# Optimization experiments

Hardware: AMD Instinct MI355X
Metric: run time of the kernel (lower is better)

Reference implementation:

```python
import jax, jax.numpy as jnp
import numpy as np

B, S, D, H = 4, 2048, 512, 8
DH = D // H


def setup_inputs() -> dict:
    key = jax.random.key(0)
    ks = jax.random.split(key, 7)
    scale = 1.0 / np.sqrt(DH)  # mimic nn.Linear init magnitude
    return {
        "x": jax.random.normal(ks[0], (B, S, D), dtype=jnp.float32),
        "Wq": jax.random.normal(ks[1], (H, DH, DH), dtype=jnp.float32) * scale,
        "bq": jax.random.normal(ks[2], (H, DH), dtype=jnp.float32) * scale,
        "Wk": jax.random.normal(ks[3], (H, DH, DH), dtype=jnp.float32) * scale,
        "bk": jax.random.normal(ks[4], (H, DH), dtype=jnp.float32) * scale,
        "Wv": jax.random.normal(ks[5], (H, DH, DH), dtype=jnp.float32) * scale,
        "bv": jax.random.normal(ks[6], (H, DH), dtype=jnp.float32) * scale,
    }


def reference(x, Wq, bq, Wk, bk, Wv, bv):
    # x: [B, S, D] -> per-head slices [B, S, H, DH] (contiguous chunks, as in torch slicing)
    xh = x.reshape(B, S, H, DH)
    # nn.Linear: y = x @ W.T + b, per head. Wq[h] is [out, in].
    q = jnp.einsum("bshd,hed->bshe", xh, Wq) + bq  # [B, S, H, DH]
    k = jnp.einsum("bshd,hed->bshe", xh, Wk) + bk
    v = jnp.einsum("bshd,hed->bshe", xh, Wv) + bv
    scores = jnp.einsum("bshe,bthe->bhst", q, k) / jnp.sqrt(jnp.float32(DH))  # [B, H, S, S]
    attn = jax.nn.softmax(scores, axis=-1)
    out = jnp.einsum("bhst,bthe->bshe", attn, v)  # [B, S, H, DH]
    return out.reshape(B, S, D)  # hstack of head outputs == concat along feature dim
```

## Files before the change

### kernel.cpp

```cpp
#include <hip/hip_runtime.h>
#include <math.h>

#define B_ 4
#define S_ 2048
#define D_ 512
#define H_ 8
#define DH_ 64
#define BH_ (B_*H_)
#define SCALE 0.1803368801111243f

typedef __attribute__((ext_vector_type(4)))  float f32x4;
typedef __attribute__((ext_vector_type(16))) float f32x16;
typedef __attribute__((ext_vector_type(8)))  short bf16x8;
typedef __attribute__((ext_vector_type(4)))  uint  u32x4;

__device__ inline uint rnepk(float a, float b) {
    uint ua = __builtin_bit_cast(uint, a), ub = __builtin_bit_cast(uint, b);
    ua += 0x7FFFu + ((ua >> 16) & 1u);
    ub += 0x7FFFu + ((ub >> 16) & 1u);
    return (ua >> 16) | (ub & 0xFFFF0000u);
}
__device__ inline uint truncpk(float lo, float hi) {
    return __builtin_amdgcn_perm(__builtin_bit_cast(uint, hi),
                                 __builtin_bit_cast(uint, lo), 0x07060302u);
}
__device__ inline f32x16 zero16() {
    f32x16 z;
    #pragma unroll
    for (int i = 0; i < 16; ++i) z[i] = 0.f;
    return z;
}
__device__ inline bf16x8 pack8(f32x4 a, f32x4 c) {
    u32x4 u;
    u.x = rnepk(a[0], a[1]); u.y = rnepk(a[2], a[3]);
    u.z = rnepk(c[0], c[1]); u.w = rnepk(c[2], c[3]);
    return __builtin_bit_cast(bf16x8, u);
}

#if __has_builtin(__builtin_amdgcn_permlane32_swap)
__device__ inline void lane32swap(uint& a, uint& b) {
    typedef __attribute__((ext_vector_type(2))) uint u32x2;
    u32x2 r = __builtin_amdgcn_permlane32_swap(a, b, false, false);
    a = r.x; b = r.y;
}
#else
__device__ inline void lane32swap(uint& a, uint& b) {
    const int l5 = (threadIdx.x & 63) >> 5;
    uint send = l5 ? a : b;
    uint recv = __shfl_xor(send, 32);
    uint an = l5 ? recv : a;
    uint bn = l5 ? b : recv;
    a = an; b = bn;
}
#endif

__global__ __launch_bounds__(256)
void prep_w(const float* __restrict__ Wq, const float* __restrict__ Wk,
            const float* __restrict__ Wv, ushort* __restrict__ Wf)
{
    const int pb = blockIdx.x;
    const int proj = pb >> 3, h = pb & 7;
    const float* W = (proj == 0 ? Wq : proj == 1 ? Wk : Wv) + h * DH_ * DH_;
    #pragma unroll
    for (int it = 0; it < 2; ++it) {
        const int slot = threadIdx.x + it * 256;
        const int c = slot >> 6, lane = slot & 63;
        const int l31 = lane & 31, l5 = lane >> 5;
        const int et = c >> 2, st = c & 3;
        const float* wr = W + (et * 32 + l31) * DH_ + st * 16 + l5 * 8;
        bf16x8 v = pack8(*(const f32x4*)wr, *(const f32x4*)(wr + 4));
        *(bf16x8*)(Wf + ((size_t)pb * 8 + c) * 512 + lane * 8) = v;
    }
}

__global__ __launch_bounds__(256, 2)
void qkv_mfma(const float* __restrict__ x,
              const float* __restrict__ bq, const float* __restrict__ bk,
              const float* __restrict__ bv, const ushort* __restrict__ Wf,
              ushort* __restrict__ Qf, ushort* __restrict__ Kf,
              ushort* __restrict__ Vf)
{
    const int bh = blockIdx.x, b = bh >> 3, h = bh & 7;
    const int sblk = blockIdx.y, s0 = sblk * 128;
    const int tid = threadIdx.x;
    const int w = tid >> 6, lane = tid & 63, l31 = lane & 31, l5 = lane >> 5;

    __shared__ __align__(16) ushort bnc[4][2560];
    __shared__ __align__(16) ushort vsh[64 * 136];
    ushort* mybnc = bnc[w];

    const ushort* wqb = Wf + ((size_t)(0 * 8 + h)) * 8 * 512;
    const ushort* wkb = Wf + ((size_t)(1 * 8 + h)) * 8 * 512;
    const ushort* wvb = Wf + ((size_t)(2 * 8 + h)) * 8 * 512;

    const int srow = w * 32 + l31;
    const float* xr = x + ((size_t)(b * S_ + s0 + srow)) * D_ + h * DH_;
    bf16x8 xf[4];
    #pragma unroll
    for (int st = 0; st < 4; ++st)
        xf[st] = pack8(*(const f32x4*)(xr + st * 16 + l5 * 8),
                       *(const f32x4*)(xr + st * 16 + l5 * 8 + 4));

    {
        bf16x8 wf[2][4];
        #pragma unroll
        for (int et = 0; et < 2; ++et)
            #pragma unroll
            for (int st = 0; st < 4; ++st)
                wf[et][st] = *(const bf16x8*)(wkb + (et * 4 + st) * 512 + lane * 8);
        #pragma unroll
        for (int et = 0; et < 2; ++et) {
            f32x16 acc = zero16();
            #pragma unroll
            for (int st = 0; st < 4; ++st)
                acc = __builtin_amdgcn_mfma_f32_32x32x16_bf16(wf[et][st], xf[st], acc, 0, 0, 0);
            #pragma unroll
            for (int rg = 0; rg < 4; ++rg) {
                float4 b4 = *(const float4*)(bk + h * DH_ + et * 32 + rg * 8 + l5 * 4);
                uint2 pk;
                pk.x = rnepk(acc[rg * 4 + 0] + b4.x, acc[rg * 4 + 1] + b4.y);
                pk.y = rnepk(acc[rg * 4 + 2] + b4.z, acc[rg * 4 + 3] + b4.w);
                *(uint2*)(mybnc + l31 * 72 + et * 32 + rg * 8 + l5 * 4) = pk;
            }
        }
        const int kt = sblk * 2 + (w >> 1), g = w & 1;
        ushort* kd = Kf + (((size_t)(bh * 32 + kt)) * 2 + g) * 2048;
        #pragma unroll
        for (int st = 0; st < 4; ++st) {
            uint4 v = *(const uint4*)(mybnc + l31 * 72 + st * 16 + l5 * 8);
            *(uint4*)(kd + st * 512 + lane * 8) = v;
        }
    }

    {
        bf16x8 wf[2][4];
        #pragma unroll
        for (int et = 0; et < 2; ++et)
            #pragma unroll
            for (int st = 0; st < 4; ++st)
                wf[et][st] = *(const bf16x8*)(wqb + (et * 4 + st) * 512 + lane * 8);
        #pragma unroll
        for (int et = 0; et < 2; ++et) {
            f32x16 acc = zero16();
            #pragma unroll
            for (int st = 0; st < 4; ++st)
                acc = __builtin_amdgcn_mfma_f32_32x32x16_bf16(wf[et][st], xf[st], acc, 0, 0, 0);
            #pragma unroll
            for (int rg = 0; rg < 4; ++rg) {
                float4 b4 = *(const float4*)(bq + h * DH_ + et * 32 + rg * 8 + l5 * 4);
                uint2 pk;
                pk.x = rnepk((acc[rg * 4 + 0] + b4.x) * SCALE, (acc[rg * 4 + 1] + b4.y) * SCALE);
                pk.y = rnepk((acc[rg * 4 + 2] + b4.z) * SCALE, (acc[rg * 4 + 3] + b4.w) * SCALE);
                *(uint2*)(mybnc + l31 * 72 + et * 32 + rg * 8 + l5 * 4) = pk;
            }
        }
        ushort* qd = Qf + ((size_t)(bh * 64 + sblk * 4 + w)) * 2048;
        #pragma unroll
        for (int st = 0; st < 4; ++st) {
            uint4 v = *(const uint4*)(mybnc + l31 * 72 + st * 16 + l5 * 8);
            *(uint4*)(qd + st * 512 + lane * 8) = v;
        }
    }

    {
        bf16x8 wf[2][4];
        #pragma unroll
        for (int et = 0; et < 2; ++et)
            #pragma unroll
            for (int st = 0; st < 4; ++st)
                wf[et][st] = *(const bf16x8*)(wvb + (et * 4 + st) * 512 + lane * 8);
        #pragma unroll
        for (int et = 0; et < 2; ++et) {
            f32x16 acc = zero16();
            #pragma unroll
            for (int st = 0; st < 4; ++st)
                acc = __builtin_amdgcn_mfma_f32_32x32x16_bf16(xf[st], wf[et][st], acc, 0, 0, 0);
            const float bb = bv[h * DH_ + et * 32 + l31];
            #pragma unroll
            for (int rg = 0; rg < 4; ++rg) {
                uint2 pk;
                pk.x = rnepk(acc[rg * 4 + 0] + bb, acc[rg * 4 + 1] + bb);
                pk.y = rnepk(acc[rg * 4 + 2] + bb, acc[rg * 4 + 3] + bb);
                *(uint2*)(vsh + (et * 32 + l31) * 136 + w * 32 + rg * 8 + l5 * 4) = pk;
            }
        }
        __syncthreads();
        #pragma unroll
        for (int i = 0; i < 4; ++i) {
            const int c = w * 4 + i;
            const int ktl = c >> 3, dht = (c >> 2) & 1, st = c & 3;
            uint4 v = *(const uint4*)(vsh + (dht * 32 + l31) * 136 + ktl * 64 + st * 16 + l5 * 8);
            *(uint4*)(Vf + (((size_t)(bh * 32 + sblk * 2 + ktl)) * 2 + dht) * 2048
                      + st * 512 + lane * 8) = v;
        }
    }
}

__global__ __launch_bounds__(256, 4)
void flash_mfma(const ushort* __restrict__ Qf, const ushort* __restrict__ Kf,
                const ushort* __restrict__ Vf, float* __restrict__ out)
{
    const int bh = blockIdx.x, qblk2 = blockIdx.y;
    const int b = bh >> 3, h = bh & 7;
    const int tid = threadIdx.x;
    const int w = tid >> 6, lane = tid & 63, l31 = lane & 31, l5 = lane >> 5;
    const int qh = w >> 1, p = w & 1;

    __shared__ __align__(16) float mb[2 * 32 * 68 + 64];

    const ushort* kbase = Kf + (size_t)bh * 32 * 4096;
    const ushort* vbase = Vf + (size_t)bh * 32 * 4096;

    bf16x8 qf[4];
    #pragma unroll
    for (int st = 0; st < 4; ++st)
        qf[st] = *(const bf16x8*)(Qf + ((size_t)(bh * 64 + qblk2 * 2 + qh)) * 2048
                                  + st * 512 + lane * 8);

    f32x16 O[2];
    O[0] = zero16(); O[1] = zero16();
    float lsum = 0.f;

    for (int step = 0; step < 16; ++step) {
        const int kt = 2 * step + p;
        const ushort* ktile = kbase + (size_t)kt * 4096;
        const ushort* vtile = vbase + (size_t)kt * 4096;

        bf16x8 pf[4];
        #pragma unroll
        for (int g = 0; g < 2; ++g) {
            bf16x8 kf[4];
            #pragma unroll
            for (int st = 0; st < 4; ++st)
                kf[st] = *(const bf16x8*)(ktile + (g * 4 + st) * 512 + lane * 8);
            f32x16 sc_ = zero16();
            __builtin_amdgcn_s_setprio(1);
            #pragma unroll
            for (int st = 0; st < 4; ++st)
                sc_ = __builtin_amdgcn_mfma_f32_32x32x16_bf16(kf[st], qf[st], sc_, 0, 0, 0);
            __builtin_amdgcn_s_setprio(0);
            uint pr[8];
            #pragma unroll
            for (int rg = 0; rg < 4; ++rg) {
                float p0 = __builtin_amdgcn_exp2f(sc_[rg * 4 + 0]);
                float p1 = __builtin_amdgcn_exp2f(sc_[rg * 4 + 1]);
                float p2 = __builtin_amdgcn_exp2f(sc_[rg * 4 + 2]);
                float p3 = __builtin_amdgcn_exp2f(sc_[rg * 4 + 3]);
                lsum += (p0 + p1) + (p2 + p3);
                pr[2 * rg + 0] = truncpk(p0, p1);
                pr[2 * rg + 1] = truncpk(p2, p3);
            }
            #pragma unroll
            for (int pp = 0; pp < 2; ++pp) {
                lane32swap(pr[4 * pp + 0], pr[4 * pp + 2]);
                lane32swap(pr[4 * pp + 1], pr[4 * pp + 3]);
                u32x4 u; u.x = pr[4 * pp + 0]; u.y = pr[4 * pp + 1];
                u.z = pr[4 * pp + 2]; u.w = pr[4 * pp + 3];
                pf[g * 2 + pp] = __builtin_bit_cast(bf16x8, u);
            }
        }

        #pragma unroll
        for (int dht = 0; dht < 2; ++dht) {
            bf16x8 vf[4];
            #pragma unroll
            for (int st = 0; st < 4; ++st)
                vf[st] = *(const bf16x8*)(vtile + (dht * 4 + st) * 512 + lane * 8);
            __builtin_amdgcn_s_setprio(1);
            #pragma unroll
            for (int st = 0; st < 4; ++st)
                O[dht] = __builtin_amdgcn_mfma_f32_32x32x16_bf16(vf[st], pf[st], O[dht], 0, 0, 0);
            __builtin_amdgcn_s_setprio(0);
        }
    }

    lsum += __shfl_xor(lsum, 32);

    float* reg = mb + qh * 2176;
    float* lsA = mb + 2 * 2176;

    if (p == 1) {
        #pragma unroll
        for (int dht = 0; dht < 2; ++dht)
            #pragma unroll
            for (int rg = 0; rg < 4; ++rg) {
                f32x4 v4;
                v4[0] = O[dht][rg * 4 + 0];
                v4[1] = O[dht][rg * 4 + 1];
                v4[2] = O[dht][rg * 4 + 2];
                v4[3] = O[dht][rg * 4 + 3];
                *(f32x4*)(reg + l31 * 68 + dht * 32 + rg * 8 + l5 * 4) = v4;
            }
        if (l5 == 0) lsA[qh * 32 + l31] = lsum;
    }
    __syncthreads();
    if (p == 0) {
        const float linv = 1.0f / (lsum + lsA[qh * 32 + l31]);
        #pragma unroll
        for (int dht = 0; dht < 2; ++dht)
            #pragma unroll
            for (int rg = 0; rg < 4; ++rg) {
                float* a = reg + l31 * 68 + dht * 32 + rg * 8 + l5 * 4;
                f32x4 part = *(const f32x4*)a;
                f32x4 v4;
                v4[0] = (O[dht][rg * 4 + 0] + part[0]) * linv;
                v4[1] = (O[dht][rg * 4 + 1] + part[1]) * linv;
                v4[2] = (O[dht][rg * 4 + 2] + part[2]) * linv;
                v4[3] = (O[dht][rg * 4 + 3] + part[3]) * linv;
                *(f32x4*)a = v4;
            }
    }
    __syncthreads();

    const int q0 = qblk2 * 64;
    #pragma unroll
    for (int i = 0; i < 4; ++i) {
        const int slot = tid + 256 * i;
        const int r = slot >> 4, c = slot & 15;
        f32x4 v = *(const f32x4*)(mb + (r >> 5) * 2176 + (r & 31) * 68 + c * 4);
        *(f32x4*)(out + ((size_t)(b * S_ + q0 + r)) * D_ + h * DH_ + c * 4) = v;
    }
}

extern "C" void kernel_launch(void* const* d_in, const int* in_sizes, int n_in,
                              void* d_out, int out_size, void* d_ws, size_t ws_size,
                              hipStream_t stream) {
    const float* x  = (const float*)d_in[0];
    const float* Wq = (const float*)d_in[1];
    const float* bq = (const float*)d_in[2];
    const float* Wk = (const float*)d_in[3];
    const float* bk = (const float*)d_in[4];
    const float* Wv = (const float*)d_in[5];
    const float* bv = (const float*)d_in[6];
    float* outp = (float*)d_out;

    ushort* Qf  = (ushort*)d_ws;
    ushort* Kf  = Qf + (size_t)BH_ * S_ * DH_;
    ushort* Vf  = Kf + (size_t)BH_ * S_ * DH_;
    ushort* Wfb = Vf + (size_t)BH_ * S_ * DH_;

    prep_w<<<dim3(24), 256, 0, stream>>>(Wq, Wk, Wv, Wfb);
    qkv_mfma<<<dim3(BH_, S_ / 128), 256, 0, stream>>>(x, bq, bk, bv, Wfb,
                                                      Qf, Kf, Vf);
    flash_mfma<<<dim3(BH_, 32), 256, 0, stream>>>(Qf, Kf, Vf, outp);
}
```

Measured before the change: 129.9 us.

## Stage K/V tiles in LDS via async global_load_lds double buffering

The flash kernel moves to 512-thread blocks covering 128 queries, with four query waves per key-split half. K and V tiles are now copied into LDS with global_load_lds DMA, double-buffered, so each tile is loaded once per block and shared by all waves instead of each wave reading it from global memory. This cuts redundant global/L2 traffic and overlaps the next tile's load with compute, at the cost of a block barrier per step, 64KB of LDS, and half as many blocks.

```diff
diff --git a/kernel.cpp b/kernel.cpp
--- a/kernel.cpp
+++ b/kernel.cpp
@@ -53,6 +53,12 @@
     a = an; b = bn;
 }
 #endif
+
+__device__ inline void dma16(const ushort* g, ushort* l) {
+    __builtin_amdgcn_global_load_lds(
+        (const __attribute__((address_space(1))) unsigned int*)g,
+        (__attribute__((address_space(3))) unsigned int*)l, 16, 0, 0);
+}
 
 __global__ __launch_bounds__(256)
 void prep_w(const float* __restrict__ Wq, const float* __restrict__ Wk,
@@ -196,25 +202,34 @@
     }
 }
 
-__global__ __launch_bounds__(256, 4)
+__global__ __launch_bounds__(512, 4)
 void flash_mfma(const ushort* __restrict__ Qf, const ushort* __restrict__ Kf,
                 const ushort* __restrict__ Vf, float* __restrict__ out)
 {
-    const int bh = blockIdx.x, qblk2 = blockIdx.y;
+    const int bh = blockIdx.x, qblk = blockIdx.y;
     const int b = bh >> 3, h = bh & 7;
     const int tid = threadIdx.x;
     const int w = tid >> 6, lane = tid & 63, l31 = lane & 31, l5 = lane >> 5;
-    const int qh = w >> 1, p = w & 1;
-
-    __shared__ __align__(16) float mb[2 * 32 * 68 + 64];
-
-    const ushort* kbase = Kf + (size_t)bh * 32 * 4096;
-    const ushort* vbase = Vf + (size_t)bh * 32 * 4096;
+    const int qi = w & 3, p = w >> 2;
+
+    __shared__ __align__(16) ushort lds_u[32768];
+
+    const ushort* gsrc = (((w >> 1) & 1) ? Vf : Kf)
+                         + (size_t)bh * 32 * 4096 + (size_t)(w & 1) * 2048;
+    const int stp = w >> 2;
+    ushort* const stdst0 = lds_u + w * 2048;
+
+    {
+        const ushort* gb = gsrc + (size_t)stp * 4096;
+        #pragma unroll
+        for (int i = 0; i < 4; ++i)
+            dma16(gb + i * 512 + lane * 8, stdst0 + i * 512);
+    }
 
     bf16x8 qf[4];
     #pragma unroll
     for (int st = 0; st < 4; ++st)
-        qf[st] = *(const bf16x8*)(Qf + ((size_t)(bh * 64 + qblk2 * 2 + qh)) * 2048
+        qf[st] = *(const bf16x8*)(Qf + ((size_t)(bh * 64 + qblk * 4 + qi)) * 2048
                                   + st * 512 + lane * 8);
 
     f32x16 O[2];
@@ -222,9 +237,17 @@
     float lsum = 0.f;
 
     for (int step = 0; step < 16; ++step) {
-        const int kt = 2 * step + p;
-        const ushort* ktile = kbase + (size_t)kt * 4096;
-        const ushort* vtile = vbase + (size_t)kt * 4096;
+        __syncthreads();
+        const ushort* cbuf = lds_u + (step & 1) * 16384;
+        if (step < 15) {
+            const ushort* gb = gsrc + (size_t)(2 * (step + 1) + stp) * 4096;
+            ushort* ld = lds_u + ((step + 1) & 1) * 16384 + w * 2048;
+            #pragma unroll
+            for (int i = 0; i < 4; ++i)
+                dma16(gb + i * 512 + lane * 8, ld + i * 512);
+        }
+        const ushort* kreg = cbuf + p * 8192;
+        const ushort* vreg = kreg + 4096;
 
         bf16x8 pf[4];
         #pragma unroll
@@ -232,7 +255,7 @@
             bf16x8 kf[4];
             #pragma unroll
             for (int st = 0; st < 4; ++st)
-                kf[st] = *(const bf16x8*)(ktile + (g * 4 + st) * 512 + lane * 8);
+                kf[st] = *(const bf16x8*)(kreg + (g * 4 + st) * 512 + lane * 8);
             f32x16 sc_ = zero16();
             __builtin_amdgcn_s_setprio(1);
             #pragma unroll
@@ -265,7 +288,7 @@
             bf16x8 vf[4];
             #pragma unroll
             for (int st = 0; st < 4; ++st)
-                vf[st] = *(const bf16x8*)(vtile + (dht * 4 + st) * 512 + lane * 8);
+                vf[st] = *(const bf16x8*)(vreg + (dht * 4 + st) * 512 + lane * 8);
             __builtin_amdgcn_s_setprio(1);
             #pragma unroll
             for (int st = 0; st < 4; ++st)
@@ -276,8 +299,10 @@
 
     lsum += __shfl_xor(lsum, 32);
 
-    float* reg = mb + qh * 2176;
-    float* lsA = mb + 2 * 2176;
+    __syncthreads();
+    float* mb = (float*)lds_u;
+    float* reg = mb + qi * 2176;
+    float* lsA = mb + 4 * 2176;
 
     if (p == 1) {
         #pragma unroll
@@ -291,11 +316,11 @@
                 v4[3] = O[dht][rg * 4 + 3];
                 *(f32x4*)(reg + l31 * 68 + dht * 32 + rg * 8 + l5 * 4) = v4;
             }
-        if (l5 == 0) lsA[qh * 32 + l31] = lsum;
+        if (l5 == 0) lsA[qi * 32 + l31] = lsum;
     }
     __syncthreads();
     if (p == 0) {
-        const float linv = 1.0f / (lsum + lsA[qh * 32 + l31]);
+        const float linv = 1.0f / (lsum + lsA[qi * 32 + l31]);
         #pragma unroll
         for (int dht = 0; dht < 2; ++dht)
             #pragma unroll
@@ -312,10 +337,10 @@
     }
     __syncthreads();
 
-    const int q0 = qblk2 * 64;
+    const int q0 = qblk * 128;
     #pragma unroll
     for (int i = 0; i < 4; ++i) {
-        const int slot = tid + 256 * i;
+        const int slot = tid + 512 * i;
         const int r = slot >> 4, c = slot & 15;
         f32x4 v = *(const f32x4*)(mb + (r >> 5) * 2176 + (r & 31) * 68 + c * 4);
         *(f32x4*)(out + ((size_t)(b * S_ + q0 + r)) * D_ + h * DH_ + c * 4) = v;
@@ -342,5 +367,5 @@
     prep_w<<<dim3(24), 256, 0, stream>>>(Wq, Wk, Wv, Wfb);
     qkv_mfma<<<dim3(BH_, S_ / 128), 256, 0, stream>>>(x, bq, bk, bv, Wfb,
                                                       Qf, Kf, Vf);
-    flash_mfma<<<dim3(BH_, 32), 256, 0, stream>>>(Qf, Kf, Vf, outp);
-}
+    flash_mfma<<<dim3(BH_, 16), 512, 0, stream>>>(Qf, Kf, Vf, outp);
+}
```

Result: faster. 126.0 us (-3.0%).
